# Performance work log

Hardware: AMD Instinct MI355X
Metric: run time of the kernel (lower is better)

The kernel has to match this reference:

```python
import jax, jax.numpy as jnp
import numpy as np

N_ATOMS = 50000
DEG = 16                 # uniform neighbor count per atom
N_EDGES = N_ATOMS * DEG
NUM_ELEMENTS = 3
NUM_PAIRS = 6
EPS = 1e-12


def setup_inputs() -> dict:
    key = jax.random.key(0)
    k0, k1, k2, k3, k4 = jax.random.split(key, 5)
    positions = jax.random.normal(k0, (N_ATOMS, 3), jnp.float32) * 10.0
    # Uniform-degree edge list: every atom i is the source of exactly DEG edges.
    source = jnp.repeat(jnp.arange(N_ATOMS, dtype=jnp.int32), DEG)
    target = jax.random.randint(k1, (N_EDGES,), 0, N_ATOMS, jnp.int32)
    edge_index = jnp.stack([source, target])          # (2, E)
    element_indices = jax.random.randint(k2, (N_ATOMS,), 0, NUM_ELEMENTS, jnp.int32)
    # symmetric element-pair -> pair-index table
    plt = np.zeros((NUM_ELEMENTS, NUM_ELEMENTS), dtype=np.int32)
    p = 0
    for a in range(NUM_ELEMENTS):
        for b in range(a, NUM_ELEMENTS):
            plt[a, b] = plt[b, a] = p
            p += 1
    pair_lookup_table = jnp.asarray(plt)
    k_angle = jax.random.uniform(k3, (NUM_PAIRS,), jnp.float32) + 0.5
    cos0 = jax.random.uniform(k4, (NUM_PAIRS,), jnp.float32) * 2.0 - 1.0
    return {
        "positions": positions,
        "edge_index": edge_index,
        "element_indices": element_indices,
        "pair_lookup_table": pair_lookup_table,
        "k_angle": k_angle,
        "cos0": cos0,
        "num_atoms": N_ATOMS,
    }


def build_triplets(edge_index, num_atoms, max_deg):
    """Vectorized, jit-compatible version of ManyBodyPotential.build_triplets.

    Returns padded triplet arrays of shape (num_atoms*max_deg*max_deg,) plus a
    validity mask; valid entries match the torch per-atom-loop output exactly.
    """
    source, target = edge_index[0], edge_index[1]
    n_edges = source.shape[0]
    sort_idx = jnp.argsort(source, stable=True)       # CSR grouping by source
    sorted_target = target[sort_idx]
    counts = jax.ops.segment_sum(jnp.ones_like(source), source,
                                 num_segments=num_atoms)          # (N,)
    row_ptr = jnp.concatenate([jnp.zeros((1,), counts.dtype),
                               jnp.cumsum(counts)])               # (N+1,)
    slot = jnp.arange(max_deg, dtype=jnp.int32)
    gidx = row_ptr[:-1, None] + slot[None, :]          # (N, MAX_DEG)
    valid = slot[None, :] < counts[:, None]            # (N, MAX_DEG)
    safe = jnp.clip(gidx, 0, n_edges - 1)
    neigh_t = sorted_target[safe]                      # (N, MAX_DEG) neighbor atom ids
    neigh_e = sort_idx[safe].astype(jnp.int32)         # (N, MAX_DEG) original edge ids
    gj, gk = jnp.meshgrid(slot, slot, indexing='ij')   # (MAX_DEG, MAX_DEG)
    pair_ok = gj != gk
    mask = valid[:, gj] & valid[:, gk] & pair_ok[None]  # (N, MD, MD)
    tj = neigh_t[:, gj]
    tk = neigh_t[:, gk]
    eij = neigh_e[:, gj]
    eik = neigh_e[:, gk]
    ti = jnp.broadcast_to(jnp.arange(num_atoms, dtype=jnp.int32)[:, None, None],
                          mask.shape)
    flat = lambda a: a.reshape(-1)
    return flat(ti), flat(tj), flat(tk), flat(eij), flat(eik), flat(mask)


def reference(positions, edge_index, element_indices, pair_lookup_table,
              k_angle, cos0, num_atoms):
    ti, tj, tk, eij, eik, mask = build_triplets(edge_index, num_atoms, DEG)
    # Angular three-body energy: sum_t k_p * (cos(theta_jik) - cos0_p)^2
    r_ij = positions[tj] - positions[ti]               # (T, 3)
    r_ik = positions[tk] - positions[ti]               # (T, 3)
    dot = jnp.sum(r_ij * r_ik, axis=-1)
    n_ij = jnp.sqrt(jnp.sum(r_ij * r_ij, axis=-1))
    n_ik = jnp.sqrt(jnp.sum(r_ik * r_ik, axis=-1))
    cos_t = dot / (n_ij * n_ik + EPS)
    p = pair_lookup_table[element_indices[tj], element_indices[tk]]
    e_t = k_angle[p] * (cos_t - cos0[p]) ** 2
    energy = jnp.sum(jnp.where(mask, e_t, 0.0))
    return energy
```

## Files before the change

### kernel.cpp

```cpp
#include <hip/hip_runtime.h>

#define DEG 16
#define ATOMS_PER_BLOCK 16

__global__ __launch_bounds__(256) void mbp_pack_kernel(
    const float* __restrict__ pos, const int* __restrict__ elem,
    float4* __restrict__ pack4, int n_atoms)
{
    const int i = blockIdx.x * 256 + threadIdx.x;
    if (i < n_atoms) {
        pack4[i] = make_float4(pos[i * 3 + 0], pos[i * 3 + 1], pos[i * 3 + 2],
                               (float)elem[i]);
    }
}

__global__ __launch_bounds__(256) void ManyBodyPotential_85143431675992_kernel(
    const float4* __restrict__ pack4,
    const int*    __restrict__ target,
    const int*    __restrict__ plt,
    const float*  __restrict__ k_angle,
    const float*  __restrict__ cos0,
    float*        __restrict__ partials,
    int n_atoms)
{
    __shared__ float  ka_tab[9];
    __shared__ float  c0_tab[9];
    __shared__ float4 s4[ATOMS_PER_BLOCK][DEG + 1];
    __shared__ float  wsum[4];

    const int t = threadIdx.x;
    if (t < 9) {
        const int p = plt[t];
        ka_tab[t] = k_angle[p];
        c0_tab[t] = cos0[p];
    }

    const int a    = t >> 4;
    const int j    = t & 15;
    const int atom = blockIdx.x * ATOMS_PER_BLOCK + a;
    const bool active = (atom < n_atoms);

    float ux = 0.f, uy = 0.f, uz = 0.f;
    int   ej = 0;
    if (active) {
        const float4 me = pack4[atom];
        const int    tj = target[atom * DEG + j];
        const float4 nb = pack4[tj];
        const float dx = nb.x - me.x;
        const float dy = nb.y - me.y;
        const float dz = nb.z - me.z;
        const float r2 = dx * dx + dy * dy + dz * dz;
        const float rinv = (r2 > 0.f) ? rsqrtf(r2) : 0.f;
        ux = dx * rinv; uy = dy * rinv; uz = dz * rinv;
        ej = (int)nb.w;
        s4[a][j] = make_float4(ux, uy, uz, nb.w);
    }
    __syncthreads();

    float acc = 0.0f;
    if (active) {
        const int   r   = ej * 3;
        const float ka0 = ka_tab[r + 0], ka1 = ka_tab[r + 1], ka2 = ka_tab[r + 2];
        const float c00 = c0_tab[r + 0], c01 = c0_tab[r + 1], c02 = c0_tab[r + 2];

        float acc2 = 0.0f, acc8 = 0.0f;
        #pragma unroll
        for (int d = 1; d <= 8; ++d) {
            const int    k  = (j + d) & 15;
            const float4 o  = s4[a][k];
            const float  ka = (o.w == 1.0f) ? ka1 : ((o.w == 2.0f) ? ka2 : ka0);
            const float  c0 = (o.w == 1.0f) ? c01 : ((o.w == 2.0f) ? c02 : c00);
            const float  ct = ux * o.x + uy * o.y + uz * o.z;
            const float  dd = ct - c0;
            const float  e  = ka * dd * dd;
            if (d < 8) acc2 += e; else acc8 = e;
        }
        acc = 2.0f * acc2 + acc8;
    }

    #pragma unroll
    for (int off = 32; off > 0; off >>= 1)
        acc += __shfl_down(acc, off, 64);
    if ((t & 63) == 0) wsum[t >> 6] = acc;
    __syncthreads();
    if (t == 0) {
        partials[blockIdx.x] = wsum[0] + wsum[1] + wsum[2] + wsum[3];
    }
}

__global__ __launch_bounds__(1024) void mbp_reduce_kernel(
    const float* __restrict__ partials, float* __restrict__ out, int n)
{
    __shared__ float wsum[16];
    const int t = threadIdx.x;
    float acc = 0.0f;
    for (int i = t; i < n; i += 1024) acc += partials[i];
    #pragma unroll
    for (int off = 32; off > 0; off >>= 1)
        acc += __shfl_down(acc, off, 64);
    if ((t & 63) == 0) wsum[t >> 6] = acc;
    __syncthreads();
    if (t == 0) {
        float s = 0.0f;
        #pragma unroll
        for (int i = 0; i < 16; ++i) s += wsum[i];
        out[0] = s;
    }
}

__global__ void mbp_zero_kernel(float* out) {
    if (threadIdx.x == 0) out[0] = 0.0f;
}

__global__ __launch_bounds__(256) void mbp_fallback_kernel(
    const float* __restrict__ pos, const int* __restrict__ target,
    const int* __restrict__ elem, const int* __restrict__ plt,
    const float* __restrict__ k_angle, const float* __restrict__ cos0,
    float* __restrict__ out, int n_atoms)
{
    __shared__ float  ka_tab[9];
    __shared__ float  c0_tab[9];
    __shared__ float4 s4[ATOMS_PER_BLOCK][DEG + 1];
    __shared__ float  wsum[4];
    const int t = threadIdx.x;
    if (t < 9) { const int p = plt[t]; ka_tab[t] = k_angle[p]; c0_tab[t] = cos0[p]; }
    const int a = t >> 4, j = t & 15;
    const int atom = blockIdx.x * ATOMS_PER_BLOCK + a;
    const bool active = (atom < n_atoms);
    float ux = 0.f, uy = 0.f, uz = 0.f; int ej = 0;
    if (active) {
        const float pix = pos[atom * 3], piy = pos[atom * 3 + 1], piz = pos[atom * 3 + 2];
        const int tj = target[atom * DEG + j];
        const float dx = pos[tj * 3] - pix, dy = pos[tj * 3 + 1] - piy, dz = pos[tj * 3 + 2] - piz;
        const float r2 = dx * dx + dy * dy + dz * dz;
        const float rinv = (r2 > 0.f) ? rsqrtf(r2) : 0.f;
        ux = dx * rinv; uy = dy * rinv; uz = dz * rinv;
        ej = elem[tj];
        s4[a][j] = make_float4(ux, uy, uz, (float)ej);
    }
    __syncthreads();
    float acc = 0.0f;
    if (active) {
        const int r = ej * 3;
        const float ka0 = ka_tab[r], ka1 = ka_tab[r + 1], ka2 = ka_tab[r + 2];
        const float c00 = c0_tab[r], c01 = c0_tab[r + 1], c02 = c0_tab[r + 2];
        float acc2 = 0.f, acc8 = 0.f;
        #pragma unroll
        for (int d = 1; d <= 8; ++d) {
            const int k = (j + d) & 15;
            const float4 o = s4[a][k];
            const float ka = (o.w == 1.0f) ? ka1 : ((o.w == 2.0f) ? ka2 : ka0);
            const float c0 = (o.w == 1.0f) ? c01 : ((o.w == 2.0f) ? c02 : c00);
            const float ct = ux * o.x + uy * o.y + uz * o.z;
            const float dd = ct - c0;
            const float e = ka * dd * dd;
            if (d < 8) acc2 += e; else acc8 = e;
        }
        acc = 2.0f * acc2 + acc8;
    }
    #pragma unroll
    for (int off = 32; off > 0; off >>= 1) acc += __shfl_down(acc, off, 64);
    if ((t & 63) == 0) wsum[t >> 6] = acc;
    __syncthreads();
    if (t == 0) atomicAdd(out, wsum[0] + wsum[1] + wsum[2] + wsum[3]);
}

extern "C" void kernel_launch(void* const* d_in, const int* in_sizes, int n_in,
                              void* d_out, int out_size, void* d_ws, size_t ws_size,
                              hipStream_t stream) {
    const float* pos     = (const float*)d_in[0];
    const int*   edge    = (const int*)d_in[1];
    const int*   elem    = (const int*)d_in[2];
    const int*   plt     = (const int*)d_in[3];
    const float* k_angle = (const float*)d_in[4];
    const float* cos0    = (const float*)d_in[5];
    float*       out     = (float*)d_out;

    const int n_atoms = in_sizes[0] / 3;
    const int n_edges = in_sizes[1] / 2;
    const int* target = edge + n_edges;

    const int n_blocks   = (n_atoms + ATOMS_PER_BLOCK - 1) / ATOMS_PER_BLOCK;
    const int pack_pad   = ((n_atoms + 255) / 256) * 256;
    const size_t need    = (size_t)pack_pad * sizeof(float4)
                         + (size_t)n_blocks * sizeof(float);
    const bool ws_ok = (d_ws != nullptr) && (ws_size >= need);

    if (ws_ok) {
        float4* pack4    = (float4*)d_ws;
        float*  partials = (float*)((char*)d_ws + (size_t)pack_pad * sizeof(float4));

        mbp_pack_kernel<<<(n_atoms + 255) / 256, 256, 0, stream>>>(
            pos, elem, pack4, n_atoms);
        ManyBodyPotential_85143431675992_kernel<<<n_blocks, 256, 0, stream>>>(
            pack4, target, plt, k_angle, cos0, partials, n_atoms);
        mbp_reduce_kernel<<<1, 1024, 0, stream>>>(partials, out, n_blocks);
    } else {
        mbp_zero_kernel<<<1, 64, 0, stream>>>(out);
        mbp_fallback_kernel<<<n_blocks, 256, 0, stream>>>(
            pos, target, elem, plt, k_angle, cos0, out, n_atoms);
    }
}
```

Measured before the change: 79.88 us.

## Fuse pack, triplet energy and final reduction into one cooperative kernel

Drops the separate position/element packing kernel and reads positions and elements straight from the inputs. Each thread now handles four neighbor edges of an atom, with 64 atoms per block, loading the four targets with one vectorized int4 load. The final partial-sum reduction moves into the same kernel behind a cooperative grid-wide sync, so three launches become one. In exchange it depends on cooperative launch support and all blocks being co-resident, pays the cost of a grid barrier, and does more uncoalesced scalar gathers per thread.

```diff
diff --git a/kernel.cpp b/kernel.cpp
--- a/kernel.cpp
+++ b/kernel.cpp
@@ -1,31 +1,25 @@
 #include <hip/hip_runtime.h>
+#include <hip/hip_cooperative_groups.h>
 
 #define DEG 16
-#define ATOMS_PER_BLOCK 16
-
-__global__ __launch_bounds__(256) void mbp_pack_kernel(
-    const float* __restrict__ pos, const int* __restrict__ elem,
-    float4* __restrict__ pack4, int n_atoms)
-{
-    const int i = blockIdx.x * 256 + threadIdx.x;
-    if (i < n_atoms) {
-        pack4[i] = make_float4(pos[i * 3 + 0], pos[i * 3 + 1], pos[i * 3 + 2],
-                               (float)elem[i]);
-    }
-}
-
-__global__ __launch_bounds__(256) void ManyBodyPotential_85143431675992_kernel(
-    const float4* __restrict__ pack4,
-    const int*    __restrict__ target,
-    const int*    __restrict__ plt,
-    const float*  __restrict__ k_angle,
-    const float*  __restrict__ cos0,
-    float*        __restrict__ partials,
-    int n_atoms)
+#define APB 64
+#define TPB 256
+#define EPS_F 1e-12f
+
+__global__ __launch_bounds__(TPB) void ManyBodyPotential_85143431675992_kernel(
+    const float* __restrict__ pos,
+    const int*   __restrict__ target,
+    const int*   __restrict__ elem,
+    const int*   __restrict__ plt,
+    const float* __restrict__ k_angle,
+    const float* __restrict__ cos0,
+    float*       __restrict__ partials,
+    float*       __restrict__ out,
+    int n_atoms, int n_blocks)
 {
     __shared__ float  ka_tab[9];
     __shared__ float  c0_tab[9];
-    __shared__ float4 s4[ATOMS_PER_BLOCK][DEG + 1];
+    __shared__ float4 s4[APB][DEG + 1];
     __shared__ float  wsum[4];
 
     const int t = threadIdx.x;
@@ -35,45 +29,53 @@
         c0_tab[t] = cos0[p];
     }
 
-    const int a    = t >> 4;
-    const int j    = t & 15;
-    const int atom = blockIdx.x * ATOMS_PER_BLOCK + a;
+    const int a    = t >> 2;
+    const int q    = t & 3;
+    const int atom = blockIdx.x * APB + a;
     const bool active = (atom < n_atoms);
 
-    float ux = 0.f, uy = 0.f, uz = 0.f;
-    int   ej = 0;
-    if (active) {
-        const float4 me = pack4[atom];
-        const int    tj = target[atom * DEG + j];
-        const float4 nb = pack4[tj];
-        const float dx = nb.x - me.x;
-        const float dy = nb.y - me.y;
-        const float dz = nb.z - me.z;
-        const float r2 = dx * dx + dy * dy + dz * dz;
-        const float rinv = (r2 > 0.f) ? rsqrtf(r2) : 0.f;
-        ux = dx * rinv; uy = dy * rinv; uz = dz * rinv;
-        ej = (int)nb.w;
-        s4[a][j] = make_float4(ux, uy, uz, nb.w);
+    float ux[4], uy[4], uz[4];
+    int   ej[4] = {0, 0, 0, 0};
+    if (active) {
+        const float pix = pos[atom * 3 + 0];
+        const float piy = pos[atom * 3 + 1];
+        const float piz = pos[atom * 3 + 2];
+        const int4 tj4 = *(const int4*)(target + atom * DEG + q * 4);
+        const int tj[4] = { tj4.x, tj4.y, tj4.z, tj4.w };
+        #pragma unroll
+        for (int e = 0; e < 4; ++e) {
+            const int   n  = tj[e];
+            const float dx = pos[n * 3 + 0] - pix;
+            const float dy = pos[n * 3 + 1] - piy;
+            const float dz = pos[n * 3 + 2] - piz;
+            const float r2 = dx * dx + dy * dy + dz * dz;
+            const float ri = (r2 > 0.f) ? rsqrtf(r2) : 0.f;
+            ux[e] = dx * ri; uy[e] = dy * ri; uz[e] = dz * ri;
+            ej[e] = elem[n];
+            s4[a][q * 4 + e] = make_float4(ux[e], uy[e], uz[e], (float)ej[e]);
+        }
     }
     __syncthreads();
 
     float acc = 0.0f;
     if (active) {
-        const int   r   = ej * 3;
-        const float ka0 = ka_tab[r + 0], ka1 = ka_tab[r + 1], ka2 = ka_tab[r + 2];
-        const float c00 = c0_tab[r + 0], c01 = c0_tab[r + 1], c02 = c0_tab[r + 2];
-
         float acc2 = 0.0f, acc8 = 0.0f;
         #pragma unroll
-        for (int d = 1; d <= 8; ++d) {
-            const int    k  = (j + d) & 15;
-            const float4 o  = s4[a][k];
-            const float  ka = (o.w == 1.0f) ? ka1 : ((o.w == 2.0f) ? ka2 : ka0);
-            const float  c0 = (o.w == 1.0f) ? c01 : ((o.w == 2.0f) ? c02 : c00);
-            const float  ct = ux * o.x + uy * o.y + uz * o.z;
-            const float  dd = ct - c0;
-            const float  e  = ka * dd * dd;
-            if (d < 8) acc2 += e; else acc8 = e;
+        for (int e = 0; e < 4; ++e) {
+            const int   j   = q * 4 + e;
+            const int   r   = ej[e] * 3;
+            const float ka0 = ka_tab[r + 0], ka1 = ka_tab[r + 1], ka2 = ka_tab[r + 2];
+            const float c00 = c0_tab[r + 0], c01 = c0_tab[r + 1], c02 = c0_tab[r + 2];
+            #pragma unroll
+            for (int d = 1; d <= 8; ++d) {
+                const float4 o  = s4[a][(j + d) & 15];
+                const float  ka = (o.w == 1.0f) ? ka1 : ((o.w == 2.0f) ? ka2 : ka0);
+                const float  c0 = (o.w == 1.0f) ? c01 : ((o.w == 2.0f) ? c02 : c00);
+                const float  ct = ux[e] * o.x + uy[e] * o.y + uz[e] * o.z;
+                const float  dd = ct - c0;
+                const float  en = ka * dd * dd;
+                if (d < 8) acc2 += en; else acc8 += en;
+            }
         }
         acc = 2.0f * acc2 + acc8;
     }
@@ -83,28 +85,21 @@
         acc += __shfl_down(acc, off, 64);
     if ((t & 63) == 0) wsum[t >> 6] = acc;
     __syncthreads();
-    if (t == 0) {
+    if (t == 0)
         partials[blockIdx.x] = wsum[0] + wsum[1] + wsum[2] + wsum[3];
-    }
-}
-
-__global__ __launch_bounds__(1024) void mbp_reduce_kernel(
-    const float* __restrict__ partials, float* __restrict__ out, int n)
-{
-    __shared__ float wsum[16];
-    const int t = threadIdx.x;
-    float acc = 0.0f;
-    for (int i = t; i < n; i += 1024) acc += partials[i];
-    #pragma unroll
-    for (int off = 32; off > 0; off >>= 1)
-        acc += __shfl_down(acc, off, 64);
-    if ((t & 63) == 0) wsum[t >> 6] = acc;
-    __syncthreads();
-    if (t == 0) {
+
+    cooperative_groups::this_grid().sync();
+
+    if (blockIdx.x == 0) {
         float s = 0.0f;
-        #pragma unroll
-        for (int i = 0; i < 16; ++i) s += wsum[i];
-        out[0] = s;
+        for (int i = t; i < n_blocks; i += TPB) s += partials[i];
+        #pragma unroll
+        for (int off = 32; off > 0; off >>= 1)
+            s += __shfl_down(s, off, 64);
+        __syncthreads();
+        if ((t & 63) == 0) wsum[t >> 6] = s;
+        __syncthreads();
+        if (t == 0) out[0] = wsum[0] + wsum[1] + wsum[2] + wsum[3];
     }
 }
 
@@ -120,12 +115,12 @@
 {
     __shared__ float  ka_tab[9];
     __shared__ float  c0_tab[9];
-    __shared__ float4 s4[ATOMS_PER_BLOCK][DEG + 1];
+    __shared__ float4 s4[16][DEG + 1];
     __shared__ float  wsum[4];
     const int t = threadIdx.x;
     if (t < 9) { const int p = plt[t]; ka_tab[t] = k_angle[p]; c0_tab[t] = cos0[p]; }
     const int a = t >> 4, j = t & 15;
-    const int atom = blockIdx.x * ATOMS_PER_BLOCK + a;
+    const int atom = blockIdx.x * 16 + a;
     const bool active = (atom < n_atoms);
     float ux = 0.f, uy = 0.f, uz = 0.f; int ej = 0;
     if (active) {
@@ -133,8 +128,8 @@
         const int tj = target[atom * DEG + j];
         const float dx = pos[tj * 3] - pix, dy = pos[tj * 3 + 1] - piy, dz = pos[tj * 3 + 2] - piz;
         const float r2 = dx * dx + dy * dy + dz * dz;
-        const float rinv = (r2 > 0.f) ? rsqrtf(r2) : 0.f;
-        ux = dx * rinv; uy = dy * rinv; uz = dz * rinv;
+        const float ri = (r2 > 0.f) ? rsqrtf(r2) : 0.f;
+        ux = dx * ri; uy = dy * ri; uz = dz * ri;
         ej = elem[tj];
         s4[a][j] = make_float4(ux, uy, uz, (float)ej);
     }
@@ -153,8 +148,8 @@
             const float c0 = (o.w == 1.0f) ? c01 : ((o.w == 2.0f) ? c02 : c00);
             const float ct = ux * o.x + uy * o.y + uz * o.z;
             const float dd = ct - c0;
-            const float e = ka * dd * dd;
-            if (d < 8) acc2 += e; else acc8 = e;
+            const float en = ka * dd * dd;
+            if (d < 8) acc2 += en; else acc8 = en;
         }
         acc = 2.0f * acc2 + acc8;
     }
@@ -180,24 +175,27 @@
     const int n_edges = in_sizes[1] / 2;
     const int* target = edge + n_edges;
 
-    const int n_blocks   = (n_atoms + ATOMS_PER_BLOCK - 1) / ATOMS_PER_BLOCK;
-    const int pack_pad   = ((n_atoms + 255) / 256) * 256;
-    const size_t need    = (size_t)pack_pad * sizeof(float4)
-                         + (size_t)n_blocks * sizeof(float);
-    const bool ws_ok = (d_ws != nullptr) && (ws_size >= need);
-
+    const int n_blocks = (n_atoms + APB - 1) / APB;
+    const bool ws_ok = (d_ws != nullptr) &&
+                       (ws_size >= (size_t)n_blocks * sizeof(float));
+
+    hipError_t err = hipErrorUnknown;
     if (ws_ok) {
-        float4* pack4    = (float4*)d_ws;
-        float*  partials = (float*)((char*)d_ws + (size_t)pack_pad * sizeof(float4));
-
-        mbp_pack_kernel<<<(n_atoms + 255) / 256, 256, 0, stream>>>(
-            pos, elem, pack4, n_atoms);
-        ManyBodyPotential_85143431675992_kernel<<<n_blocks, 256, 0, stream>>>(
-            pack4, target, plt, k_angle, cos0, partials, n_atoms);
-        mbp_reduce_kernel<<<1, 1024, 0, stream>>>(partials, out, n_blocks);
-    } else {
+        float* partials = (float*)d_ws;
+        void* args[] = {
+            (void*)&pos, (void*)&target, (void*)&elem, (void*)&plt,
+            (void*)&k_angle, (void*)&cos0, (void*)&partials, (void*)&out,
+            (void*)&n_atoms, (void*)&n_blocks
+        };
+        err = hipLaunchCooperativeKernel(
+            (const void*)ManyBodyPotential_85143431675992_kernel,
+            dim3(n_blocks), dim3(TPB), args, 0, stream);
+    }
+
+    if (err != hipSuccess) {
+        const int fb_blocks = (n_atoms + 15) / 16;
         mbp_zero_kernel<<<1, 64, 0, stream>>>(out);
-        mbp_fallback_kernel<<<n_blocks, 256, 0, stream>>>(
+        mbp_fallback_kernel<<<fb_blocks, 256, 0, stream>>>(
             pos, target, elem, plt, k_angle, cos0, out, n_atoms);
     }
 }
```

Result: slower. 170.2 us (+113.0%).
